# Performance work log

Hardware: AMD Instinct MI355X
Metric: run time of the kernel (lower is better)

The kernel has to match this reference:

```python
import jax, jax.numpy as jnp
import numpy as np

N, G, E = 100000, 32768, 1000000
F, H = 64, 64


def _mlp(x, w1, b1, w2, b2):
    # Linear -> SiLU -> Linear (matches nn.Sequential in the torch module)
    return jax.nn.silu(x @ w1 + b1) @ w2 + b2


def setup_inputs() -> dict:
    key = jax.random.key(0)
    ks = jax.random.split(key, 24)

    def lin(k, fan_in, fan_out):
        s = 1.0 / np.sqrt(fan_in)
        kw, kb = jax.random.split(k)
        w = jax.random.uniform(kw, (fan_in, fan_out), jnp.float32, -s, s)
        b = jax.random.uniform(kb, (fan_out,), jnp.float32, -s, s)
        return w, b

    node_w1, node_b1 = lin(ks[0], F, H)
    node_w2, node_b2 = lin(ks[1], H, H)
    edge_w1, edge_b1 = lin(ks[2], 6, H)
    edge_w2, edge_b2 = lin(ks[3], H, H)
    msg_w1, msg_b1 = lin(ks[4], 2 * H, H)
    msg_w2, msg_b2 = lin(ks[5], H, H)
    upd_w1, upd_b1 = lin(ks[6], H, H)
    upd_w2, upd_b2 = lin(ks[7], H, H)

    return {
        "node_features": jax.random.normal(ks[8], (N, F), jnp.float32),
        "node_pos": jax.random.normal(ks[9], (N, 3), jnp.float32),
        "grid_pos": jax.random.normal(ks[10], (G, 3), jnp.float32),
        "orientations": jax.random.normal(ks[11], (N, 3, 3), jnp.float32),
        "edge_index": jnp.stack([
            jax.random.randint(ks[12], (E,), 0, N),
            jax.random.randint(ks[13], (E,), 0, G),
        ]),
        "node_w1": node_w1, "node_b1": node_b1, "node_w2": node_w2, "node_b2": node_b2,
        "edge_w1": edge_w1, "edge_b1": edge_b1, "edge_w2": edge_w2, "edge_b2": edge_b2,
        "msg_w1": msg_w1, "msg_b1": msg_b1, "msg_w2": msg_w2, "msg_b2": msg_b2,
        "upd_w1": upd_w1, "upd_b1": upd_b1, "upd_w2": upd_w2, "upd_b2": upd_b2,
    }


def reference(node_features, node_pos, grid_pos, orientations, edge_index,
              node_w1, node_b1, node_w2, node_b2,
              edge_w1, edge_b1, edge_w2, edge_b2,
              msg_w1, msg_b1, msg_w2, msg_b2,
              upd_w1, upd_b1, upd_w2, upd_b2):
    source, target = edge_index[0], edge_index[1]
    num_grid = grid_pos.shape[0]

    # node MLP
    h_node = _mlp(node_features, node_w1, node_b1, node_w2, node_b2)  # [N,H]

    # per-edge message with orientation-aware projection
    pos_s = node_pos[source]                 # [E,3]
    rel = grid_pos[target] - pos_s           # [E,3]
    # bmm(rel[:,None,:], R[source]).squeeze(1) == einsum ei,eij->ej
    trel = jnp.einsum("ei,eij->ej", rel, orientations[source])
    edge_attr = jnp.concatenate([pos_s, trel], axis=-1)        # [E,6]
    e_feat = _mlp(edge_attr, edge_w1, edge_b1, edge_w2, edge_b2)
    msg_in = jnp.concatenate([h_node[source], e_feat], axis=-1)  # [E,2H]
    messages = _mlp(msg_in, msg_w1, msg_b1, msg_w2, msg_b2)      # [E,H]

    # scatter-mean into grid buckets (mask out-of-range targets)
    valid = (target >= 0) & (target < num_grid)
    idx = jnp.where(valid, target, 0)
    msg_masked = jnp.where(valid[:, None], messages, 0.0)
    sums = jax.ops.segment_sum(msg_masked, idx, num_segments=num_grid)
    cnts = jax.ops.segment_sum(valid.astype(jnp.float32), idx, num_segments=num_grid)
    grid_feat = sums / jnp.maximum(cnts, 1.0)[:, None]

    return _mlp(grid_feat, upd_w1, upd_b1, upd_w2, upd_b2)  # [G,H]
```

## Files before the change

### kernel.cpp

```cpp
#include <hip/hip_runtime.h>
#include <hip/hip_bf16.h>
#include <cstdint>

typedef __attribute__((ext_vector_type(8))) short short8;
typedef __attribute__((ext_vector_type(4))) float f32x4;
typedef unsigned short u16;

__device__ __forceinline__ float b2f(u16 u) {
  union { unsigned int i; float f; } v; v.i = ((unsigned int)u) << 16; return v.f;
}
__device__ __forceinline__ u16 f2b(float f) {
  __hip_bfloat16 h = __float2bfloat16(f);
  union { __hip_bfloat16 h; u16 u; } v; v.h = h; return v.u;
}
__device__ __forceinline__ float silu_f(float x) { return x / (1.0f + __expf(-x)); }

__device__ __forceinline__ float loadF(const void* p, long i, int isf32) {
  if (isf32) return ((const float*)p)[i];
  return b2f(((const u16*)p)[i]);
}

__device__ __forceinline__ int sniffbit(u16 u) {
  unsigned e = (u >> 7) & 0xffu;
  return (e >= 0xC0u || (e < 0x40u && (u & 0x7fffu) != 0)) ? 1 : 0;
}

struct Ptrs { const void* p[20]; int n[20]; };

#define FW_EW1 0
#define FW_UW1 384
#define FW_UW2 4480
#define FW_UB1 8576
#define FW_UB2 8640
#define FW_EB1 8704
#define FW_EB2 8768
#define FW_MB1 8832
#define FW_MB2 8896
#define FW_TOTAL 8960

#define IMG_EW2 0
#define IMG_MW1 4608
#define IMG_MW2 13312
#define IMG_TOTAL 17920

#define PREP_BLOCKS 105
#define HIST_BLOCKS 1024

__global__ __launch_bounds__(256) void hist_detect_k(
    Ptrs a, const int* __restrict__ eidx, int* __restrict__ cnt8,
    int* __restrict__ flags, long E, int G)
{
  const int t = threadIdx.x;
  const int b = blockIdx.x;
  if (b < HIST_BLOCKS) {
    int* cs = cnt8 + (size_t)(b & 7) * G;
    long i = (long)b * 256 + t;
    const long stride = (long)HIST_BLOCKS * 256;
    for (; i < E; i += stride) {
      int tg = eidx[E + i];
      if (tg >= 0 && tg < G) atomicAdd(&cs[tg], 1);
    }
    return;
  }
  int j = b - HIST_BLOCKS;
  const u16* q = (const u16*)a.p[j];
  int n = a.n[j];
  int m = n < 4096 ? n : 4096;
  int cnt = 0;
  for (int i = t; i < m; i += 256) cnt += sniffbit(q[i]);
  __shared__ int tot;
  if (t == 0) tot = 0;
  __syncthreads();
  if (cnt) atomicAdd(&tot, cnt);
  __syncthreads();
  if (t == 0) flags[j] = (tot >= 2) ? 1 : 0;
}

__global__ __launch_bounds__(256) void scan_prep_node_k(
    Ptrs a, const int* __restrict__ flags,
    const int* __restrict__ cnt8, int* __restrict__ cursor8,
    int* __restrict__ bsum,
    u16* __restrict__ img, float* __restrict__ fw,
    u16* __restrict__ hout, int nrows, int G, int NB2)
{
  const int t = threadIdx.x;
  const int b = blockIdx.x;

  if (b < NB2) {
    __shared__ int sd[256];
    const long tot = 8L * G;
    long j0 = (long)b * 1024 + (long)t * 4;
    int v[4];
#pragma unroll
    for (int k = 0; k < 4; ++k) {
      long j = j0 + k;
      v[k] = (j < tot) ? cnt8[(size_t)(j & 7) * G + (j >> 3)] : 0;
    }
    int local = v[0] + v[1] + v[2] + v[3];
    sd[t] = local;
    __syncthreads();
    for (int off = 1; off < 256; off <<= 1) {
      int x2 = (t >= off) ? sd[t - off] : 0;
      __syncthreads();
      sd[t] += x2;
      __syncthreads();
    }
    int p = sd[t] - local;
#pragma unroll
    for (int k = 0; k < 4; ++k) {
      long j = j0 + k;
      if (j < tot) cursor8[(size_t)(j & 7) * G + (j >> 3)] = p;
      p += v[k];
    }
    if (t == 255) bsum[b] = sd[255];
    return;
  }

  if (b < NB2 + PREP_BLOCKS) {
    int i = (b - NB2) * 256 + t;
    if (i < IMG_TOTAL) {
      const void* bp; int fl; long si; bool real;
      if (i < IMG_MW1) { int nn = i / 72, k = i % 72; bp = a.p[10]; fl = flags[10]; real = k < 64; si = (long)k * 64 + nn; }
      else if (i < IMG_MW2) { int t2 = i - IMG_MW1; int nn = t2 / 136, k = t2 % 136; bp = a.p[12]; fl = flags[12]; real = k < 128; si = (long)k * 64 + nn; }
      else { int t2 = i - IMG_MW2; int nn = t2 / 72, k = t2 % 72; bp = a.p[14]; fl = flags[14]; real = k < 64; si = (long)k * 64 + nn; }
      u16 val = 0;
      if (real) val = f2b(loadF(bp, si, fl));
      img[i] = val;
    } else if (i < IMG_TOTAL + FW_TOTAL) {
      int j = i - IMG_TOTAL;
      const void* bp; int fl; long si;
      if (j < 384)        { bp = a.p[8];  fl = flags[8];  si = j; }
      else if (j < 4480)  { bp = a.p[16]; fl = flags[16]; si = j - 384; }
      else if (j < 8576)  { bp = a.p[18]; fl = flags[18]; si = j - 4480; }
      else {
        int bb = j - 8576; int seg = bb >> 6; si = bb & 63;
        switch (seg) {
          case 0: bp = a.p[17]; fl = flags[17]; break;
          case 1: bp = a.p[19]; fl = flags[19]; break;
          case 2: bp = a.p[9];  fl = flags[9];  break;
          case 3: bp = a.p[11]; fl = flags[11]; break;
          case 4: bp = a.p[13]; fl = flags[13]; break;
          default: bp = a.p[15]; fl = flags[15]; break;
        }
      }
      fw[j] = loadF(bp, si, fl);
    }
    return;
  }

  __shared__ float xs[64][68];
  __shared__ float w1s[64][68];
  __shared__ float w2s[64][68];
  __shared__ float b1s[64];
  __shared__ float b2s[64];
  const void* x = a.p[0];
  const int xf = flags[0], f1 = flags[4], fb1 = flags[5], f2 = flags[6], fb2 = flags[7];
  const long rbase = (long)(b - NB2 - PREP_BLOCKS) * 64;
  for (int i = t; i < 4096; i += 256) {
    int k = i >> 6, cc = i & 63;
    w1s[k][cc] = loadF(a.p[4], i, f1);
    w2s[k][cc] = loadF(a.p[6], i, f2);
  }
  if (t < 64) { b1s[t] = loadF(a.p[5], t, fb1); b2s[t] = loadF(a.p[7], t, fb2); }
  {
    int row = t >> 2, ch = t & 3;
    long rg = rbase + row;
    if (rg < nrows) {
      if (xf) {
        const float* xp = (const float*)x + rg * 64 + ch * 16;
#pragma unroll
        for (int m = 0; m < 16; ++m) xs[row][ch * 16 + m] = xp[m];
      } else {
        const u16* xp = (const u16*)x + rg * 64 + ch * 16;
#pragma unroll
        for (int m = 0; m < 16; ++m) xs[row][ch * 16 + m] = b2f(xp[m]);
      }
    } else {
#pragma unroll
      for (int m = 0; m < 16; ++m) xs[row][ch * 16 + m] = 0.f;
    }
  }
  __syncthreads();
  const int r0 = (t >> 4) * 4, c0 = (t & 15) * 4;
  float acc[4][4];
#pragma unroll
  for (int i = 0; i < 4; ++i)
#pragma unroll
    for (int j = 0; j < 4; ++j) acc[i][j] = b1s[c0 + j];
  for (int k = 0; k < 64; ++k) {
    float w0 = w1s[k][c0], w1v = w1s[k][c0 + 1], w2v = w1s[k][c0 + 2], w3v = w1s[k][c0 + 3];
#pragma unroll
    for (int i = 0; i < 4; ++i) {
      float av = xs[r0 + i][k];
      acc[i][0] = fmaf(av, w0, acc[i][0]);
      acc[i][1] = fmaf(av, w1v, acc[i][1]);
      acc[i][2] = fmaf(av, w2v, acc[i][2]);
      acc[i][3] = fmaf(av, w3v, acc[i][3]);
    }
  }
  __syncthreads();
#pragma unroll
  for (int i = 0; i < 4; ++i)
#pragma unroll
    for (int j = 0; j < 4; ++j) xs[r0 + i][c0 + j] = silu_f(acc[i][j]);
  __syncthreads();
  float acc2[4][4];
#pragma unroll
  for (int i = 0; i < 4; ++i)
#pragma unroll
    for (int j = 0; j < 4; ++j) acc2[i][j] = b2s[c0 + j];
  for (int k = 0; k < 64; ++k) {
    float w0 = w2s[k][c0], w1v = w2s[k][c0 + 1], w2v = w2s[k][c0 + 2], w3v = w2s[k][c0 + 3];
#pragma unroll
    for (int i = 0; i < 4; ++i) {
      float av = xs[r0 + i][k];
      acc2[i][0] = fmaf(av, w0, acc2[i][0]);
      acc2[i][1] = fmaf(av, w1v, acc2[i][1]);
      acc2[i][2] = fmaf(av, w2v, acc2[i][2]);
      acc2[i][3] = fmaf(av, w3v, acc2[i][3]);
    }
  }
#pragma unroll
  for (int i = 0; i < 4; ++i) {
    long rg = rbase + r0 + i;
    if (rg < nrows) {
#pragma unroll
      for (int j = 0; j < 4; ++j) hout[rg * 64 + c0 + j] = f2b(acc2[i][j]);
    }
  }
}

__global__ __launch_bounds__(256) void scat_k(const int* __restrict__ eidx,
                                              int* __restrict__ cursor8,
                                              const int* __restrict__ bsum,
                                              unsigned int* __restrict__ pkS,
                                              int* __restrict__ evp,
                                              long E, int G, int NB2) {
  __shared__ int bo[256];
  const int t = threadIdx.x;
  int v = (t < NB2) ? bsum[t] : 0;
  bo[t] = v;
  __syncthreads();
  for (int off = 1; off < 256; off <<= 1) {
    int x2 = (t >= off) ? bo[t - off] : 0;
    __syncthreads();
    bo[t] += x2;
    __syncthreads();
  }
  if (blockIdx.x == 0 && t == 0) *evp = bo[NB2 - 1];
  int excl = bo[t] - v;
  __syncthreads();
  bo[t] = excl;
  __syncthreads();
  const int c = blockIdx.x & 7;
  int* cur = cursor8 + (size_t)c * G;
  long i = (long)blockIdx.x * 256 + t;
  const long stride = (long)gridDim.x * 256;
  for (; i < E; i += stride) {
    int tg = eidx[E + i];
    if (tg >= 0 && tg < G) {
      int s = eidx[i];
      long j = ((long)tg << 3) | c;
      int p = atomicAdd(&cur[tg], 1) + bo[j >> 10];
      __builtin_nontemporal_store((unsigned int)s | ((unsigned int)tg << 17), pkS + p);
    }
  }
}

#define ETILES 4

__global__ __launch_bounds__(256, 5) void edge_kernel(
    const void* node_pos, const void* grid_pos, const void* orient,
    const unsigned int* __restrict__ pkS, const int* __restrict__ evp,
    const u16* __restrict__ h_node, const u16* __restrict__ img,
    const float* __restrict__ fw, const int* __restrict__ flags,
    float* __restrict__ sums, int G)
{
  __shared__ __align__(16) u16 pool[4][3328];
  __shared__ float eaf[64][6];
  __shared__ float w1e[6][64];
  __shared__ float biasE[4][64];
  __shared__ int tgt_s[64];
  __shared__ int src_s[64];

  const int t = threadIdx.x;
  const int pf = flags[1], gf = flags[2], of = flags[3];
  const int Ev = *evp;
  for (int i = t; i < 384; i += 256) w1e[i / 64][i % 64] = fw[FW_EW1 + i];
  { int seg = t >> 6, cc = t & 63; biasE[seg][cc] = fw[FW_EB1 + seg * 64 + cc]; }
  __syncthreads();

  const int lane = t & 63, w = t >> 6;
  const int q = lane >> 4, c = lane & 15;
  const int m0 = w * 16;
  u16 (* __restrict__ ef1w)[72] = (u16 (*)[72])&pool[w][0];
  u16 (* __restrict__ hAw)[136] = (u16 (*)[136])&pool[w][1152];
  float (* __restrict__ msgfw)[66] = (float (*)[66])&pool[w][1152];
  const u16* wE2 = img + IMG_EW2;
  const u16* wM1 = img + IMG_MW1;
  const u16* wM2 = img + IMG_MW2;
  const f32x4 z = {0.f, 0.f, 0.f, 0.f};

  for (int tile = 0; tile < ETILES; ++tile) {
    long base = ((long)blockIdx.x * ETILES + tile) * 64;
    if (base >= Ev) break;
    if (lane < 16) {
      long eg = base + m0 + lane;
      int s = 0, tg = -1;
      if (eg < Ev) {
        unsigned int pk = pkS[eg];
        s = (int)(pk & 0x1FFFFu);
        tg = (int)(pk >> 17);
      }
      tgt_s[m0 + lane] = tg;
      src_s[m0 + lane] = s;
      int tgc = (tg >= 0) ? tg : 0;
      float ps[3], rel[3], tr[3];
#pragma unroll
      for (int i = 0; i < 3; ++i) {
        ps[i] = loadF(node_pos, (long)s * 3 + i, pf);
        rel[i] = loadF(grid_pos, (long)tgc * 3 + i, gf) - ps[i];
      }
#pragma unroll
      for (int j = 0; j < 3; ++j) tr[j] = 0.f;
#pragma unroll
      for (int i = 0; i < 3; ++i)
#pragma unroll
        for (int j = 0; j < 3; ++j)
          tr[j] = fmaf(rel[i], loadF(orient, (long)s * 9 + i * 3 + j, of), tr[j]);
      eaf[m0 + lane][0] = ps[0]; eaf[m0 + lane][1] = ps[1]; eaf[m0 + lane][2] = ps[2];
      eaf[m0 + lane][3] = tr[0]; eaf[m0 + lane][4] = tr[1]; eaf[m0 + lane][5] = tr[2];
    }
    __syncthreads();

    {
      int er = lane >> 2, ch = lane & 3;
      const u16* hp = h_node + (long)src_s[m0 + er] * 64 + ch * 16;
      short8 v0 = *(const short8*)hp;
      short8 v1 = *(const short8*)(hp + 8);
      *(short8*)&hAw[er][ch * 16] = v0;
      *(short8*)&hAw[er][ch * 16 + 8] = v1;
    }
    {
      int e = lane >> 2, c0 = (lane & 3) * 16;
      int eb = m0 + e;
      float a0 = eaf[eb][0], a1 = eaf[eb][1], a2 = eaf[eb][2];
      float a3 = eaf[eb][3], a4 = eaf[eb][4], a5 = eaf[eb][5];
      __align__(16) u16 tmp[16];
#pragma unroll
      for (int j = 0; j < 16; ++j) {
        int cc = c0 + j;
        float acc = biasE[0][cc];
        acc = fmaf(a0, w1e[0][cc], acc);
        acc = fmaf(a1, w1e[1][cc], acc);
        acc = fmaf(a2, w1e[2][cc], acc);
        acc = fmaf(a3, w1e[3][cc], acc);
        acc = fmaf(a4, w1e[4][cc], acc);
        acc = fmaf(a5, w1e[5][cc], acc);
        tmp[j] = f2b(silu_f(acc));
      }
      *(short8*)&ef1w[e][c0] = *(const short8*)tmp;
      *(short8*)&ef1w[e][c0 + 8] = *(const short8*)(tmp + 8);
    }
    __builtin_amdgcn_wave_barrier();
    {
      short8 a0 = *(const short8*)&ef1w[c][q * 8];
      short8 a1 = *(const short8*)&ef1w[c][32 + q * 8];
#pragma unroll
      for (int nt = 0; nt < 4; ++nt) {
        short8 b0 = *(const short8*)&wE2[(nt * 16 + c) * 72 + q * 8];
        short8 b1v = *(const short8*)&wE2[(nt * 16 + c) * 72 + 32 + q * 8];
        f32x4 acc = __builtin_amdgcn_mfma_f32_16x16x32_bf16(a0, b0, z, 0, 0, 0);
        acc = __builtin_amdgcn_mfma_f32_16x16x32_bf16(a1, b1v, acc, 0, 0, 0);
#pragma unroll
        for (int r = 0; r < 4; ++r) {
          int row = q * 4 + r, col = nt * 16 + c;
          hAw[row][64 + col] = f2b(acc[r] + biasE[1][col]);
        }
      }
    }
    __builtin_amdgcn_wave_barrier();
    {
      short8 a0 = *(const short8*)&hAw[c][q * 8];
      short8 a1 = *(const short8*)&hAw[c][32 + q * 8];
      short8 a2 = *(const short8*)&hAw[c][64 + q * 8];
      short8 a3 = *(const short8*)&hAw[c][96 + q * 8];
#pragma unroll
      for (int nt = 0; nt < 4; ++nt) {
        const u16* wp = &wM1[(nt * 16 + c) * 136];
        f32x4 acc = __builtin_amdgcn_mfma_f32_16x16x32_bf16(a0, *(const short8*)(wp + q * 8), z, 0, 0, 0);
        acc = __builtin_amdgcn_mfma_f32_16x16x32_bf16(a1, *(const short8*)(wp + 32 + q * 8), acc, 0, 0, 0);
        acc = __builtin_amdgcn_mfma_f32_16x16x32_bf16(a2, *(const short8*)(wp + 64 + q * 8), acc, 0, 0, 0);
        acc = __builtin_amdgcn_mfma_f32_16x16x32_bf16(a3, *(const short8*)(wp + 96 + q * 8), acc, 0, 0, 0);
#pragma unroll
        for (int r = 0; r < 4; ++r) {
          int row = q * 4 + r, col = nt * 16 + c;
          ef1w[row][col] = f2b(silu_f(acc[r] + biasE[2][col]));
        }
      }
    }
    __builtin_amdgcn_wave_barrier();
    {
      short8 a0 = *(const short8*)&ef1w[c][q * 8];
      short8 a1 = *(const short8*)&ef1w[c][32 + q * 8];
      __builtin_amdgcn_wave_barrier();
#pragma unroll
      for (int nt = 0; nt < 4; ++nt) {
        short8 b0 = *(const short8*)&wM2[(nt * 16 + c) * 72 + q * 8];
        short8 b1v = *(const short8*)&wM2[(nt * 16 + c) * 72 + 32 + q * 8];
        f32x4 acc = __builtin_amdgcn_mfma_f32_16x16x32_bf16(a0, b0, z, 0, 0, 0);
        acc = __builtin_amdgcn_mfma_f32_16x16x32_bf16(a1, b1v, acc, 0, 0, 0);
#pragma unroll
        for (int r = 0; r < 4; ++r) {
          int row = q * 4 + r, col = nt * 16 + c;
          msgfw[row][col] = acc[r] + biasE[3][col];
        }
      }
    }
    __builtin_amdgcn_wave_barrier();
    {
      int col = lane;
      int cur = tgt_s[m0];
      float run = msgfw[0][col];
      bool lopen = (m0 == 0) ? true : (tgt_s[m0 - 1] == cur);
#pragma unroll
      for (int r2 = 1; r2 < 16; ++r2) {
        int tg = tgt_s[m0 + r2];
        float v = msgfw[r2][col];
        if (tg == cur) {
          run += v;
        } else {
          if (cur >= 0) {
            if (lopen) unsafeAtomicAdd(&sums[(long)cur * 64 + col], run);
            else sums[(long)cur * 64 + col] = run;
          }
          cur = tg; run = v; lopen = false;
        }
      }
      bool ropen = (m0 + 16 >= 64) ? true : (tgt_s[m0 + 16] == cur);
      if (cur >= 0) {
        if (lopen || ropen) unsafeAtomicAdd(&sums[(long)cur * 64 + col], run);
        else sums[(long)cur * 64 + col] = run;
      }
    }
    __syncthreads();
  }
}

__global__ __launch_bounds__(256) void upd_mlp(
    const float* __restrict__ sums, const int* __restrict__ cnt8,
    const float* __restrict__ fw, float* __restrict__ out, int nrows)
{
  __shared__ float xs[64][68];
  __shared__ float w1s[64][68];
  __shared__ float w2s[64][68];
  __shared__ float b1s[64];
  __shared__ float b2s[64];
  const int t = threadIdx.x;
  const long rbase = (long)blockIdx.x * 64;
  for (int i = t; i < 4096; i += 256) {
    int k = i >> 6, cc = i & 63;
    w1s[k][cc] = fw[FW_UW1 + i];
    w2s[k][cc] = fw[FW_UW2 + i];
  }
  if (t < 64) { b1s[t] = fw[FW_UB1 + t]; b2s[t] = fw[FW_UB2 + t]; }
  {
    int row = t >> 2, ch = t & 3;
    long rg = rbase + row;
    if (rg < nrows) {
      int cn = 0;
#pragma unroll
      for (int cc = 0; cc < 8; ++cc) cn += cnt8[(size_t)cc * nrows + rg];
      float inv = 1.0f / fmaxf((float)cn, 1.0f);
      const float* p = sums + rg * 64 + ch * 16;
#pragma unroll
      for (int m = 0; m < 16; ++m) xs[row][ch * 16 + m] = p[m] * inv;
    } else {
#pragma unroll
      for (int m = 0; m < 16; ++m) xs[row][ch * 16 + m] = 0.f;
    }
  }
  __syncthreads();
  const int r0 = (t >> 4) * 4, c0 = (t & 15) * 4;
  float acc[4][4];
#pragma unroll
  for (int i = 0; i < 4; ++i)
#pragma unroll
    for (int j = 0; j < 4; ++j) acc[i][j] = b1s[c0 + j];
  for (int k = 0; k < 64; ++k) {
    float w0 = w1s[k][c0], w1v = w1s[k][c0 + 1], w2v = w1s[k][c0 + 2], w3v = w1s[k][c0 + 3];
#pragma unroll
    for (int i = 0; i < 4; ++i) {
      float av = xs[r0 + i][k];
      acc[i][0] = fmaf(av, w0, acc[i][0]);
      acc[i][1] = fmaf(av, w1v, acc[i][1]);
      acc[i][2] = fmaf(av, w2v, acc[i][2]);
      acc[i][3] = fmaf(av, w3v, acc[i][3]);
    }
  }
  __syncthreads();
#pragma unroll
  for (int i = 0; i < 4; ++i)
#pragma unroll
    for (int j = 0; j < 4; ++j) xs[r0 + i][c0 + j] = silu_f(acc[i][j]);
  __syncthreads();
  float acc2[4][4];
#pragma unroll
  for (int i = 0; i < 4; ++i)
#pragma unroll
    for (int j = 0; j < 4; ++j) acc2[i][j] = b2s[c0 + j];
  for (int k = 0; k < 64; ++k) {
    float w0 = w2s[k][c0], w1v = w2s[k][c0 + 1], w2v = w2s[k][c0 + 2], w3v = w2s[k][c0 + 3];
#pragma unroll
    for (int i = 0; i < 4; ++i) {
      float av = xs[r0 + i][k];
      acc2[i][0] = fmaf(av, w0, acc2[i][0]);
      acc2[i][1] = fmaf(av, w1v, acc2[i][1]);
      acc2[i][2] = fmaf(av, w2v, acc2[i][2]);
      acc2[i][3] = fmaf(av, w3v, acc2[i][3]);
    }
  }
#pragma unroll
  for (int i = 0; i < 4; ++i) {
    long rg = rbase + r0 + i;
    if (rg < nrows) {
#pragma unroll
      for (int j = 0; j < 4; ++j) out[rg * 64 + c0 + j] = acc2[i][j];
    }
  }
}

extern "C" void kernel_launch(void* const* d_in, const int* in_sizes, int n_in,
                              void* d_out, int out_size, void* d_ws, size_t ws_size,
                              hipStream_t stream) {
  const int N = in_sizes[1] / 3;
  const int G = in_sizes[2] / 3;
  const long E = (long)in_sizes[4] / 2;
  const int NB2 = (int)((8L * G + 1023) / 1024);
  const int nodeBlocks = (N + 63) / 64;

  char* ws = (char*)d_ws;
  float* sums = (float*)ws;
  size_t off = (size_t)G * 256;
  int* cnt8 = (int*)(ws + off);     off += (size_t)G * 32;
  int* cursor8 = (int*)(ws + off);  off += (size_t)G * 32;
  int* bsum = (int*)(ws + off);     off += 1024;
  int* evp = (int*)(ws + off);      off += 256;
  int* flags = (int*)(ws + off);    off += 256;
  unsigned int* pkS = (unsigned int*)(ws + off); off += (size_t)E * 4;
  u16* h_node = (u16*)(ws + off);   off += (size_t)N * 128;
  u16* img = (u16*)(ws + off);      off += (size_t)IMG_TOTAL * 2;
  float* fw = (float*)(ws + off);

  hipMemsetAsync(ws, 0, (size_t)G * 288, stream);

  Ptrs a;
  const int map[20] = {0,1,2,3, 5,6,7,8, 9,10,11,12, 13,14,15,16, 17,18,19,20};
  for (int i = 0; i < 20; ++i) { a.p[i] = d_in[map[i]]; a.n[i] = in_sizes[map[i]]; }

  hist_detect_k<<<HIST_BLOCKS + 20, 256, 0, stream>>>(
      a, (const int*)d_in[4], cnt8, flags, E, G);
  scan_prep_node_k<<<NB2 + PREP_BLOCKS + nodeBlocks, 256, 0, stream>>>(
      a, flags, cnt8, cursor8, bsum, img, fw, h_node, N, G, NB2);
  scat_k<<<1024, 256, 0, stream>>>((const int*)d_in[4], cursor8, bsum, pkS, evp, E, G, NB2);
  edge_kernel<<<(int)((E + ETILES * 64 - 1) / (ETILES * 64)), 256, 0, stream>>>(
      d_in[1], d_in[2], d_in[3], pkS, evp, h_node, img, fw, flags, sums, G);
  upd_mlp<<<(G + 63) / 64, 256, 0, stream>>>(sums, cnt8, fw, (float*)d_out, G);
}
```

Baseline: 464.7 us.

## Software-pipeline edge gathers across tiles and use rcp in SiLU

Packed edge indices for all tiles of a block are loaded up front. The gathers for the next tile (node_pos, grid_pos, orientations, and h_node rows via a shuffle of the packed source index) are issued before the current tile's scatter phase, so their latency overlaps with compute instead of stalling at the top of each tile. This removes the src_s shared array and moves h_node staging before the block barrier. SiLU also replaces the division with a hardware reciprocal, which is slightly less precise. The prefetched values are held in extra registers, which may lower occupancy under the launch bounds.

Result: slower. 512.2 us (+10.2%).

```diff
diff --git a/kernel.cpp b/kernel.cpp
--- a/kernel.cpp
+++ b/kernel.cpp
@@ -13,7 +13,9 @@
   __hip_bfloat16 h = __float2bfloat16(f);
   union { __hip_bfloat16 h; u16 u; } v; v.h = h; return v.u;
 }
-__device__ __forceinline__ float silu_f(float x) { return x / (1.0f + __expf(-x)); }
+__device__ __forceinline__ float silu_f(float x) {
+  return x * __builtin_amdgcn_rcpf(1.0f + __expf(-x));
+}
 
 __device__ __forceinline__ float loadF(const void* p, long i, int isf32) {
   if (isf32) return ((const float*)p)[i];
@@ -281,7 +283,6 @@
   __shared__ float w1e[6][64];
   __shared__ float biasE[4][64];
   __shared__ int tgt_s[64];
-  __shared__ int src_s[64];
 
   const int t = threadIdx.x;
   const int pf = flags[1], gf = flags[2], of = flags[3];
@@ -301,46 +302,69 @@
   const u16* wM2 = img + IMG_MW2;
   const f32x4 z = {0.f, 0.f, 0.f, 0.f};
 
+  const long blockBase = (long)blockIdx.x * (ETILES * 64);
+
+  unsigned int pkt[ETILES];
+#pragma unroll
+  for (int tn = 0; tn < ETILES; ++tn) {
+    long eg = blockBase + (long)tn * 64 + m0 + lane;
+    pkt[tn] = (lane < 16 && eg < Ev) ? pkS[eg] : 0u;
+  }
+
+  float gps[3], ggp[3], gor[9];
+  int gtg = -1;
+  short8 hv0, hv1;
+
+  auto prefetch = [&](int tn) {
+    long tb = blockBase + (long)tn * 64;
+    unsigned int pk = pkt[tn];
+    int gs = (int)(pk & 0x1FFFFu);
+    gtg = (int)(pk >> 17);
+    if (tb + m0 + lane >= Ev) { gs = 0; gtg = -1; }
+    if (lane < 16) {
+      int tgc = (gtg >= 0) ? gtg : 0;
+#pragma unroll
+      for (int i = 0; i < 3; ++i) gps[i] = loadF(node_pos, (long)gs * 3 + i, pf);
+#pragma unroll
+      for (int i = 0; i < 3; ++i) ggp[i] = loadF(grid_pos, (long)tgc * 3 + i, gf);
+#pragma unroll
+      for (int i = 0; i < 9; ++i) gor[i] = loadF(orient, (long)gs * 9 + i, of);
+    }
+    unsigned int pk2 = (unsigned int)__shfl((int)pkt[tn], lane >> 2);
+    int ss = ((tb + m0 + (lane >> 2)) < Ev) ? (int)(pk2 & 0x1FFFFu) : 0;
+    const u16* hp = h_node + (long)ss * 64 + (lane & 3) * 16;
+    hv0 = *(const short8*)hp;
+    hv1 = *(const short8*)(hp + 8);
+  };
+
+  prefetch(0);
+
+#pragma unroll
   for (int tile = 0; tile < ETILES; ++tile) {
-    long base = ((long)blockIdx.x * ETILES + tile) * 64;
+    long base = blockBase + (long)tile * 64;
     if (base >= Ev) break;
+
     if (lane < 16) {
-      long eg = base + m0 + lane;
-      int s = 0, tg = -1;
-      if (eg < Ev) {
-        unsigned int pk = pkS[eg];
-        s = (int)(pk & 0x1FFFFu);
-        tg = (int)(pk >> 17);
-      }
-      tgt_s[m0 + lane] = tg;
-      src_s[m0 + lane] = s;
-      int tgc = (tg >= 0) ? tg : 0;
-      float ps[3], rel[3], tr[3];
-#pragma unroll
-      for (int i = 0; i < 3; ++i) {
-        ps[i] = loadF(node_pos, (long)s * 3 + i, pf);
-        rel[i] = loadF(grid_pos, (long)tgc * 3 + i, gf) - ps[i];
-      }
+      tgt_s[m0 + lane] = gtg;
+      float rel[3], tr[3];
+#pragma unroll
+      for (int i = 0; i < 3; ++i) rel[i] = ggp[i] - gps[i];
 #pragma unroll
       for (int j = 0; j < 3; ++j) tr[j] = 0.f;
 #pragma unroll
       for (int i = 0; i < 3; ++i)
 #pragma unroll
-        for (int j = 0; j < 3; ++j)
-          tr[j] = fmaf(rel[i], loadF(orient, (long)s * 9 + i * 3 + j, of), tr[j]);
-      eaf[m0 + lane][0] = ps[0]; eaf[m0 + lane][1] = ps[1]; eaf[m0 + lane][2] = ps[2];
+        for (int j = 0; j < 3; ++j) tr[j] = fmaf(rel[i], gor[i * 3 + j], tr[j]);
+      eaf[m0 + lane][0] = gps[0]; eaf[m0 + lane][1] = gps[1]; eaf[m0 + lane][2] = gps[2];
       eaf[m0 + lane][3] = tr[0]; eaf[m0 + lane][4] = tr[1]; eaf[m0 + lane][5] = tr[2];
     }
-    __syncthreads();
-
     {
       int er = lane >> 2, ch = lane & 3;
-      const u16* hp = h_node + (long)src_s[m0 + er] * 64 + ch * 16;
-      short8 v0 = *(const short8*)hp;
-      short8 v1 = *(const short8*)(hp + 8);
-      *(short8*)&hAw[er][ch * 16] = v0;
-      *(short8*)&hAw[er][ch * 16 + 8] = v1;
-    }
+      *(short8*)&hAw[er][ch * 16] = hv0;
+      *(short8*)&hAw[er][ch * 16 + 8] = hv1;
+    }
+    __syncthreads();
+
     {
       int e = lane >> 2, c0 = (lane & 3) * 16;
       int eb = m0 + e;
@@ -418,6 +442,10 @@
       }
     }
     __builtin_amdgcn_wave_barrier();
+
+    __builtin_amdgcn_sched_barrier(0);
+    if (tile + 1 < ETILES && base + 64 < Ev) prefetch(tile + 1);
+
     {
       int col = lane;
       int cur = tgt_s[m0];
```

## Prefetch next tile's h_node rows into LDS via async global_load_lds

Applied to the files above, without the earlier changes.

Edge indices for all four tiles are now loaded up front and held in registers. The h_node gather for the next tile is issued as direct global-to-LDS loads while the current tile's message MLP runs, which overlaps gather latency with MFMA work. The LDS pool is re-laid out with a separate staging region and e_feat buffer, and __syncthreads is replaced by explicit waitcnt plus s_barrier. SiLU now uses a hardware reciprocal instead of a divide. In exchange the code depends on manual waitcnt ordering and a hand-managed LDS layout, which is fragile.

Result: slower. 507.7 us (+9.3%).

```diff
diff --git a/kernel.cpp b/kernel.cpp
--- a/kernel.cpp
+++ b/kernel.cpp
@@ -13,11 +13,19 @@
   __hip_bfloat16 h = __float2bfloat16(f);
   union { __hip_bfloat16 h; u16 u; } v; v.h = h; return v.u;
 }
-__device__ __forceinline__ float silu_f(float x) { return x / (1.0f + __expf(-x)); }
+__device__ __forceinline__ float silu_f(float x) {
+  return x * __builtin_amdgcn_rcpf(1.0f + __expf(-x));
+}
 
 __device__ __forceinline__ float loadF(const void* p, long i, int isf32) {
   if (isf32) return ((const float*)p)[i];
   return b2f(((const u16*)p)[i]);
+}
+
+__device__ __forceinline__ void gload_lds16(const void* g, void* l) {
+  __builtin_amdgcn_global_load_lds(
+      (const __attribute__((address_space(1))) void*)g,
+      (__attribute__((address_space(3))) void*)l, 16, 0, 0);
 }
 
 __device__ __forceinline__ int sniffbit(u16 u) {
@@ -281,66 +289,85 @@
   __shared__ float w1e[6][64];
   __shared__ float biasE[4][64];
   __shared__ int tgt_s[64];
-  __shared__ int src_s[64];
 
   const int t = threadIdx.x;
   const int pf = flags[1], gf = flags[2], of = flags[3];
   const int Ev = *evp;
-  for (int i = t; i < 384; i += 256) w1e[i / 64][i % 64] = fw[FW_EW1 + i];
-  { int seg = t >> 6, cc = t & 63; biasE[seg][cc] = fw[FW_EB1 + seg * 64 + cc]; }
-  __syncthreads();
 
   const int lane = t & 63, w = t >> 6;
   const int q = lane >> 4, c = lane & 15;
   const int m0 = w * 16;
-  u16 (* __restrict__ ef1w)[72] = (u16 (*)[72])&pool[w][0];
-  u16 (* __restrict__ hAw)[136] = (u16 (*)[136])&pool[w][1152];
-  float (* __restrict__ msgfw)[66] = (float (*)[66])&pool[w][1152];
+  u16* hstage = &pool[w][0];
+  u16 (* __restrict__ ef1w)[72] = (u16 (*)[72])&pool[w][1024];
+  u16 (* __restrict__ efeat)[72] = (u16 (*)[72])&pool[w][2176];
+  float (* __restrict__ msgfw)[66] = (float (*)[66])&pool[w][1024];
   const u16* wE2 = img + IMG_EW2;
   const u16* wM1 = img + IMG_MW1;
   const u16* wM2 = img + IMG_MW2;
   const f32x4 z = {0.f, 0.f, 0.f, 0.f};
 
+  const long blockBase = (long)blockIdx.x * (ETILES * 64);
+
+  unsigned int pkA = 0, pkB = 0, pkC = 0, pkD = 0;
+  if (lane < 16) {
+    long e0 = blockBase + m0 + lane;
+    if (e0 < Ev)       pkA = pkS[e0];
+    if (e0 + 64 < Ev)  pkB = pkS[e0 + 64];
+    if (e0 + 128 < Ev) pkC = pkS[e0 + 128];
+    if (e0 + 192 < Ev) pkD = pkS[e0 + 192];
+  }
+
+  {
+    unsigned int pks = (unsigned int)__shfl((int)pkA, lane & 15);
+    int ss = (int)(pks & 0x1FFFFu);
+    const u16* gp = h_node + (long)ss * 64 + (size_t)(lane >> 4) * 8;
+    gload_lds16(gp, hstage);
+    gload_lds16(gp + 32, hstage + 512);
+  }
+
+  for (int i = t; i < 384; i += 256) w1e[i / 64][i % 64] = fw[FW_EW1 + i];
+  { int seg = t >> 6, cc = t & 63; biasE[seg][cc] = fw[FW_EB1 + seg * 64 + cc]; }
+  __syncthreads();
+
   for (int tile = 0; tile < ETILES; ++tile) {
-    long base = ((long)blockIdx.x * ETILES + tile) * 64;
+    long base = blockBase + (long)tile * 64;
     if (base >= Ev) break;
+
+    asm volatile("s_waitcnt vmcnt(0)" ::: "memory");
+    __builtin_amdgcn_sched_barrier(0);
+
     if (lane < 16) {
       long eg = base + m0 + lane;
-      int s = 0, tg = -1;
-      if (eg < Ev) {
-        unsigned int pk = pkS[eg];
-        s = (int)(pk & 0x1FFFFu);
-        tg = (int)(pk >> 17);
-      }
+      int gs = (int)(pkA & 0x1FFFFu);
+      int tg = (eg < Ev) ? (int)(pkA >> 17) : -1;
       tgt_s[m0 + lane] = tg;
-      src_s[m0 + lane] = s;
       int tgc = (tg >= 0) ? tg : 0;
-      float ps[3], rel[3], tr[3];
-#pragma unroll
-      for (int i = 0; i < 3; ++i) {
-        ps[i] = loadF(node_pos, (long)s * 3 + i, pf);
-        rel[i] = loadF(grid_pos, (long)tgc * 3 + i, gf) - ps[i];
-      }
-#pragma unroll
-      for (int j = 0; j < 3; ++j) tr[j] = 0.f;
-#pragma unroll
-      for (int i = 0; i < 3; ++i)
-#pragma unroll
-        for (int j = 0; j < 3; ++j)
-          tr[j] = fmaf(rel[i], loadF(orient, (long)s * 9 + i * 3 + j, of), tr[j]);
-      eaf[m0 + lane][0] = ps[0]; eaf[m0 + lane][1] = ps[1]; eaf[m0 + lane][2] = ps[2];
-      eaf[m0 + lane][3] = tr[0]; eaf[m0 + lane][4] = tr[1]; eaf[m0 + lane][5] = tr[2];
-    }
-    __syncthreads();
-
-    {
-      int er = lane >> 2, ch = lane & 3;
-      const u16* hp = h_node + (long)src_s[m0 + er] * 64 + ch * 16;
-      short8 v0 = *(const short8*)hp;
-      short8 v1 = *(const short8*)(hp + 8);
-      *(short8*)&hAw[er][ch * 16] = v0;
-      *(short8*)&hAw[er][ch * 16 + 8] = v1;
-    }
+      float ps0 = loadF(node_pos, (long)gs * 3 + 0, pf);
+      float ps1 = loadF(node_pos, (long)gs * 3 + 1, pf);
+      float ps2 = loadF(node_pos, (long)gs * 3 + 2, pf);
+      float rel0 = loadF(grid_pos, (long)tgc * 3 + 0, gf) - ps0;
+      float rel1 = loadF(grid_pos, (long)tgc * 3 + 1, gf) - ps1;
+      float rel2 = loadF(grid_pos, (long)tgc * 3 + 2, gf) - ps2;
+      float o0 = loadF(orient, (long)gs * 9 + 0, of);
+      float o1 = loadF(orient, (long)gs * 9 + 1, of);
+      float o2 = loadF(orient, (long)gs * 9 + 2, of);
+      float o3 = loadF(orient, (long)gs * 9 + 3, of);
+      float o4 = loadF(orient, (long)gs * 9 + 4, of);
+      float o5 = loadF(orient, (long)gs * 9 + 5, of);
+      float o6 = loadF(orient, (long)gs * 9 + 6, of);
+      float o7 = loadF(orient, (long)gs * 9 + 7, of);
+      float o8 = loadF(orient, (long)gs * 9 + 8, of);
+      float tr0 = rel0 * o0; tr0 = fmaf(rel1, o3, tr0); tr0 = fmaf(rel2, o6, tr0);
+      float tr1 = rel0 * o1; tr1 = fmaf(rel1, o4, tr1); tr1 = fmaf(rel2, o7, tr1);
+      float tr2 = rel0 * o2; tr2 = fmaf(rel1, o5, tr2); tr2 = fmaf(rel2, o8, tr2);
+      eaf[m0 + lane][0] = ps0; eaf[m0 + lane][1] = ps1; eaf[m0 + lane][2] = ps2;
+      eaf[m0 + lane][3] = tr0; eaf[m0 + lane][4] = tr1; eaf[m0 + lane][5] = tr2;
+    }
+    __builtin_amdgcn_sched_barrier(0);
+    asm volatile("s_waitcnt lgkmcnt(0)" ::: "memory");
+    __builtin_amdgcn_s_barrier();
+    __builtin_amdgcn_sched_barrier(0);
+
     {
       int e = lane >> 2, c0 = (lane & 3) * 16;
       int eb = m0 + e;
@@ -375,16 +402,27 @@
 #pragma unroll
         for (int r = 0; r < 4; ++r) {
           int row = q * 4 + r, col = nt * 16 + c;
-          hAw[row][64 + col] = f2b(acc[r] + biasE[1][col]);
+          efeat[row][col] = f2b(acc[r] + biasE[1][col]);
         }
       }
     }
     __builtin_amdgcn_wave_barrier();
     {
-      short8 a0 = *(const short8*)&hAw[c][q * 8];
-      short8 a1 = *(const short8*)&hAw[c][32 + q * 8];
-      short8 a2 = *(const short8*)&hAw[c][64 + q * 8];
-      short8 a3 = *(const short8*)&hAw[c][96 + q * 8];
+      short8 a0 = *(const short8*)&hstage[q * 128 + c * 8];
+      short8 a1 = *(const short8*)&hstage[512 + q * 128 + c * 8];
+      short8 a2 = *(const short8*)&efeat[c][q * 8];
+      short8 a3 = *(const short8*)&efeat[c][32 + q * 8];
+      __builtin_amdgcn_sched_barrier(0);
+      asm volatile("s_waitcnt lgkmcnt(0)" ::: "memory");
+      __builtin_amdgcn_sched_barrier(0);
+      if (tile + 1 < ETILES && base + 64 < Ev) {
+        unsigned int pks = (unsigned int)__shfl((int)pkB, lane & 15);
+        int ss = (int)(pks & 0x1FFFFu);
+        const u16* gp = h_node + (long)ss * 64 + (size_t)(lane >> 4) * 8;
+        gload_lds16(gp, hstage);
+        gload_lds16(gp + 32, hstage + 512);
+      }
+      __builtin_amdgcn_sched_barrier(0);
 #pragma unroll
       for (int nt = 0; nt < 4; ++nt) {
         const u16* wp = &wM1[(nt * 16 + c) * 136];
@@ -418,6 +456,7 @@
       }
     }
     __builtin_amdgcn_wave_barrier();
+
     {
       int col = lane;
       int cur = tgt_s[m0];
@@ -443,7 +482,11 @@
         else sums[(long)cur * 64 + col] = run;
       }
     }
-    __syncthreads();
+    __builtin_amdgcn_sched_barrier(0);
+    asm volatile("s_waitcnt lgkmcnt(0)" ::: "memory");
+    __builtin_amdgcn_s_barrier();
+    __builtin_amdgcn_sched_barrier(0);
+    pkA = pkB; pkB = pkC; pkC = pkD;
   }
 }
 
```
